# Kernel tuning notes

Hardware: AMD Instinct MI355X
Metric: run time of the kernel (lower is better)

Reference implementation:

```python
import jax, jax.numpy as jnp
import numpy as np

CODEBOOK_SIZE = 1024
CODEWORD_SIZE = 256
BETA = 0.1
N_INIT = 1  # embedding ~ U(-1/n, 1/n)


def setup_inputs() -> dict:
    key = jax.random.key(0)
    kx, ke = jax.random.split(key)
    x = jax.random.normal(kx, (16, 4096, CODEWORD_SIZE), dtype=jnp.float32)
    embedding = jax.random.uniform(
        ke, (CODEBOOK_SIZE, CODEWORD_SIZE), dtype=jnp.float32,
        minval=-1.0 / N_INIT, maxval=1.0 / N_INIT)
    return {"x": x, "embedding": embedding}


def reference(x, embedding):
    dist = (jnp.sum(x * x, axis=2, keepdims=True)
            + jnp.sum(embedding * embedding, axis=1)
            - 2.0 * jnp.einsum('btd,kd->btk', x, embedding))
    indexes = jnp.argmin(dist, axis=2)              # [B,T] int
    values = jnp.take(embedding, indexes, axis=0)   # gather == one_hot @ embedding
    sg = jax.lax.stop_gradient
    loss1 = jnp.mean((sg(x) - values) ** 2)         # codebook loss
    loss2 = jnp.mean((x - sg(values)) ** 2)         # commitment loss
    loss = loss1 + BETA * loss2
    values_st = x + sg(values - x)                  # straight-through
    return values_st, indexes, loss
```

## Files before the change

### kernel.cpp

```cpp
#include <hip/hip_runtime.h>
#include <stdint.h>


#define BT    65536
#define D     256
#define KCB   1024
#define BM    256
#define BN    128
#define BK    32

typedef float    f32x4 __attribute__((ext_vector_type(4)));
typedef _Float16 f16x8 __attribute__((ext_vector_type(8)));

#define GLOAD_LDS16(g, l) \
  __builtin_amdgcn_global_load_lds((const __attribute__((address_space(1))) void*)(g), \
                                   (__attribute__((address_space(3))) void*)(l), 16, 0, 0)

__global__ __launch_bounds__(256) void split_e_kernel(const float* __restrict__ E,
                                                      _Float16* __restrict__ Eh,
                                                      _Float16* __restrict__ El,
                                                      float* __restrict__ enorm,
                                                      float* __restrict__ out_loss) {
    if (blockIdx.x == 0 && threadIdx.x == 0) *out_loss = 0.f;
    const int r = blockIdx.x * 8 + (threadIdx.x >> 5);
    const size_t i0 = (size_t)r * D + (threadIdx.x & 31) * 8;
    float4 v0 = *(const float4*)(E + i0);
    float4 v1 = *(const float4*)(E + i0 + 4);
    float v[8] = {v0.x, v0.y, v0.z, v0.w, v1.x, v1.y, v1.z, v1.w};
    f16x8 h, l;
    float s = 0.f;
    #pragma unroll
    for (int j = 0; j < 8; ++j) {
        _Float16 hh = (_Float16)v[j];
        h[j] = hh;
        l[j] = (_Float16)(v[j] - (float)hh);
        s += v[j] * v[j];
    }
    *(f16x8*)(Eh + i0) = h;
    *(f16x8*)(El + i0) = l;
    #pragma unroll
    for (int off = 1; off < 32; off <<= 1) s += __shfl_xor(s, off, 64);
    if ((threadIdx.x & 31) == 0) enorm[r] = s;
}

__global__ __launch_bounds__(512, 2) void vq_mfma_kernel(
    const float* __restrict__ X,
    const _Float16* __restrict__ Eh, const _Float16* __restrict__ El,
    const float* __restrict__ enorm, const float* __restrict__ E,
    float* __restrict__ out_vals, float* __restrict__ out_idx,
    float* __restrict__ out_loss) {
    __shared__ __align__(16) char Bmem[8 * BN * BK * 2];
    __shared__ float s_en[KCB];
    __shared__ float s_bd[BM];
    __shared__ int   s_bi[BM];
    __shared__ float s_red[8];

    float*    const Xs = (float*)Bmem;
    _Float16* const BB = (_Float16*)Bmem;

    const int tid  = threadIdx.x;
    const int w    = tid >> 6;
    const int lane = tid & 63;
    const int quad = lane >> 4;
    const int l16  = lane & 15;
    const int sxa  = l16 & 7;
    const int row0 = blockIdx.x * BM;

    const int sb_row = lane >> 2;
    const int sb_off = ((((lane & 3) - (lane >> 3)) & 3) << 3);
    const int kob = ((quad + ((l16 >> 1) & 3)) & 3) << 3;

    auto STAGE_PH = [&](int buf, int step) {
        const int col0 = (step >> 2) * BN;
        const int kb0  = (step & 3) * (2 * BK);
        #pragma unroll
        for (int h = 0; h < 2; ++h) {
            const int gr = col0 + w * 16 + sb_row;
            const size_t gb = (size_t)gr * D + kb0 + h * BK + sb_off;
            GLOAD_LDS16(Eh + gb, BB + (buf * 4 + h * 2 + 0) * (BN * BK) + w * 512);
            GLOAD_LDS16(El + gb, BB + (buf * 4 + h * 2 + 1) * (BN * BK) + w * 512);
        }
    };

    s_en[tid]       = enorm[tid];
    s_en[tid + 512] = enorm[tid + 512];

    f16x8 pah[2][8], pal[2][8];
    float xs = 0.f;
    for (int p = 0; p < 4; ++p) {
        #pragma unroll
        for (int rr = 0; rr < 8; ++rr) {
            const int sr = w * 8 + rr;
            const int gr = row0 + p * 64 + sr;
            GLOAD_LDS16(X + (size_t)gr * D + ((lane ^ rr) << 2), &Xs[sr * D]);
        }
        asm volatile("s_waitcnt vmcnt(0) lgkmcnt(0)" ::: "memory");
        __builtin_amdgcn_s_barrier();
        if ((w >> 1) == p) {
            const int srb = (w & 1) * 32;
            #pragma unroll
            for (int i = 0; i < 2; ++i) {
                const float* rp = &Xs[(srb + i * 16 + l16) * D];
                #pragma unroll
                for (int kc = 0; kc < 8; ++kc) {
                    const int c0 = kc * 8 + quad * 2;
                    const f32x4 v0 = *(const f32x4*)(rp + (((c0)     ^ sxa) << 2));
                    const f32x4 v1 = *(const f32x4*)(rp + (((c0 | 1) ^ sxa) << 2));
                    const float f[8] = {v0.x, v0.y, v0.z, v0.w, v1.x, v1.y, v1.z, v1.w};
                    #pragma unroll
                    for (int e = 0; e < 8; ++e) {
                        const _Float16 hh = (_Float16)f[e];
                        pah[i][kc][e] = hh;
                        pal[i][kc][e] = (_Float16)(f[e] - (float)hh);
                        xs += f[e] * f[e];
                    }
                }
            }
        }
        __builtin_amdgcn_s_barrier();
    }

    float rb_d[2][4];
    int   rb_i[2][4];
    #pragma unroll
    for (int i = 0; i < 2; ++i)
        #pragma unroll
        for (int r = 0; r < 4; ++r) { rb_d[i][r] = 3.4e38f; rb_i[i][r] = 0; }
    f32x4 acc[2][8];

    STAGE_PH(0, 0);
    for (int nt = 0; nt < 8; ++nt) {
        const int col0 = nt * BN;
        #pragma unroll
        for (int q = 0; q < 4; ++q) {
            const int cur = q & 1;
            if (nt == 7 && q == 3) {
                asm volatile("s_waitcnt vmcnt(0)" ::: "memory");
            } else {
                STAGE_PH(cur ^ 1, nt * 4 + q + 1);
                asm volatile("s_waitcnt vmcnt(4)" ::: "memory");
            }
            __builtin_amdgcn_s_barrier();

            if (q == 0) {
                #pragma unroll
                for (int i = 0; i < 2; ++i)
                    #pragma unroll
                    for (int j = 0; j < 8; ++j) acc[i][j] = (f32x4)0.0f;
            }

            #pragma unroll
            for (int sub = 0; sub < 2; ++sub) {
                const int kc = q * 2 + sub;
                const _Float16* Bh = BB + (cur * 4 + sub * 2 + 0) * (BN * BK);
                const _Float16* Bl = BB + (cur * 4 + sub * 2 + 1) * (BN * BK);
                __builtin_amdgcn_s_setprio(1);
                #pragma unroll
                for (int j = 0; j < 8; ++j) {
                    const int n = (j * 16 + l16) * BK + kob;
                    const f16x8 bh = *(const f16x8*)&Bh[n];
                    const f16x8 bl = *(const f16x8*)&Bl[n];
                    #pragma unroll
                    for (int i = 0; i < 2; ++i) {
                        acc[i][j] = __builtin_amdgcn_mfma_f32_16x16x32_f16(pah[i][kc], bh, acc[i][j], 0, 0, 0);
                        acc[i][j] = __builtin_amdgcn_mfma_f32_16x16x32_f16(pal[i][kc], bh, acc[i][j], 0, 0, 0);
                        acc[i][j] = __builtin_amdgcn_mfma_f32_16x16x32_f16(pah[i][kc], bl, acc[i][j], 0, 0, 0);
                    }
                }
                __builtin_amdgcn_s_setprio(0);
            }

            if (q == 3) {
                #pragma unroll
                for (int j = 0; j < 8; ++j) {
                    const int c = col0 + j * 16 + l16;
                    const float en = s_en[c];
                    #pragma unroll
                    for (int i = 0; i < 2; ++i)
                        #pragma unroll
                        for (int r = 0; r < 4; ++r) {
                            const float sd = en - 2.0f * acc[i][j][r];
                            if (sd < rb_d[i][r]) { rb_d[i][r] = sd; rb_i[i][r] = c; }
                        }
                }
            }
            __builtin_amdgcn_s_barrier();
        }
    }

    #pragma unroll
    for (int off = 1; off < 16; off <<= 1) {
        #pragma unroll
        for (int i = 0; i < 2; ++i)
            #pragma unroll
            for (int r = 0; r < 4; ++r) {
                const float od = __shfl_xor(rb_d[i][r], off, 64);
                const int   oi = __shfl_xor(rb_i[i][r], off, 64);
                if (od < rb_d[i][r] || (od == rb_d[i][r] && oi < rb_i[i][r])) {
                    rb_d[i][r] = od; rb_i[i][r] = oi;
                }
            }
    }
    if (l16 == 0) {
        #pragma unroll
        for (int i = 0; i < 2; ++i)
            #pragma unroll
            for (int r = 0; r < 4; ++r) {
                const int m = w * 32 + i * 16 + quad * 4 + r;
                s_bd[m] = rb_d[i][r]; s_bi[m] = rb_i[i][r];
            }
    }
    __syncthreads();

    float part = xs;
    if (tid < BM) {
        out_idx[row0 + tid] = (float)s_bi[tid];
        part += s_bd[tid];
    }

    const int col = tid & 255;
    const int sub = tid >> 8;
    #pragma unroll 4
    for (int it = 0; it < BM / 2; ++it) {
        const int r  = it * 2 + sub;
        const int bi = s_bi[r];
        out_vals[(size_t)(row0 + r) * D + col] = E[(size_t)bi * D + col];
    }

    #pragma unroll
    for (int off = 1; off < 64; off <<= 1) part += __shfl_xor(part, off, 64);
    if (lane == 0) s_red[w] = part;
    __syncthreads();
    if (tid == 0) {
        float tot = 0.f;
        #pragma unroll
        for (int i = 0; i < 8; ++i) tot += s_red[i];
        atomicAdd(out_loss, tot * (1.1f / 16777216.f));
    }
}

extern "C" void kernel_launch(void* const* d_in, const int* in_sizes, int n_in,
                              void* d_out, int out_size, void* d_ws, size_t ws_size,
                              hipStream_t stream) {
    const float* X = (const float*)d_in[0];
    const float* E = (const float*)d_in[1];
    float* out      = (float*)d_out;
    float* out_vals = out;
    float* out_idx  = out + (size_t)BT * D;
    float* out_loss = out + (size_t)BT * D + BT;

    char* ws = (char*)d_ws;
    _Float16* Eh    = (_Float16*)ws;
    _Float16* El    = Eh + (size_t)KCB * D;
    float*    enorm = (float*)(El + (size_t)KCB * D);
    (void)ws_size; (void)n_in; (void)in_sizes; (void)out_size;

    split_e_kernel<<<KCB / 8, 256, 0, stream>>>(E, Eh, El, enorm, out_loss);
    vq_mfma_kernel<<<BT / BM, 512, 0, stream>>>(X, Eh, El, enorm, E,
                                                out_vals, out_idx, out_loss);
}
```

Measured before the change: 189.9 us.

## Halve row tile to 128 with 4-wave blocks and double-buffer X staging

Shrinks each block to 128 rows and 256 threads (4 waves), which doubles the grid to 512 blocks. The codebook staging is split so each wave loads two chunks. X prologue loads are now double-buffered across two LDS regions so the next 32-row slab loads while the current one is converted to fp16 hi/lo fragments. The enorm load is moved to the end of the prologue. This should improve load balance over the CUs and overlap the prologue, but each block streams the full codebook for half as many rows, which doubles total codebook traffic per output row.

```diff
diff --git a/kernel.cpp b/kernel.cpp
--- a/kernel.cpp
+++ b/kernel.cpp
@@ -5,7 +5,7 @@
 #define BT    65536
 #define D     256
 #define KCB   1024
-#define BM    256
+#define BM    128
 #define BN    128
 #define BK    32
 
@@ -43,7 +43,7 @@
     if ((threadIdx.x & 31) == 0) enorm[r] = s;
 }
 
-__global__ __launch_bounds__(512, 2) void vq_mfma_kernel(
+__global__ __launch_bounds__(256, 2) void vq_mfma_kernel(
     const float* __restrict__ X,
     const _Float16* __restrict__ Eh, const _Float16* __restrict__ El,
     const float* __restrict__ enorm, const float* __restrict__ E,
@@ -53,10 +53,11 @@
     __shared__ float s_en[KCB];
     __shared__ float s_bd[BM];
     __shared__ int   s_bi[BM];
-    __shared__ float s_red[8];
-
-    float*    const Xs = (float*)Bmem;
-    _Float16* const BB = (_Float16*)Bmem;
+    __shared__ float s_red[4];
+
+    _Float16* const BB  = (_Float16*)Bmem;
+    float*    const Xs0 = (float*)Bmem;
+    float*    const Xs1 = (float*)(Bmem + 32 * 1024);
 
     const int tid  = threadIdx.x;
     const int w    = tid >> 6;
@@ -74,33 +75,47 @@
         const int col0 = (step >> 2) * BN;
         const int kb0  = (step & 3) * (2 * BK);
         #pragma unroll
-        for (int h = 0; h < 2; ++h) {
-            const int gr = col0 + w * 16 + sb_row;
-            const size_t gb = (size_t)gr * D + kb0 + h * BK + sb_off;
-            GLOAD_LDS16(Eh + gb, BB + (buf * 4 + h * 2 + 0) * (BN * BK) + w * 512);
-            GLOAD_LDS16(El + gb, BB + (buf * 4 + h * 2 + 1) * (BN * BK) + w * 512);
-        }
+        for (int h = 0; h < 2; ++h)
+            #pragma unroll
+            for (int t = 0; t < 2; ++t) {
+                const int chunk = w * 2 + t;
+                const int gr = col0 + chunk * 16 + sb_row;
+                const size_t gb = (size_t)gr * D + kb0 + h * BK + sb_off;
+                GLOAD_LDS16(Eh + gb, BB + (buf * 4 + h * 2 + 0) * (BN * BK) + chunk * 512);
+                GLOAD_LDS16(El + gb, BB + (buf * 4 + h * 2 + 1) * (BN * BK) + chunk * 512);
+            }
     };
 
-    s_en[tid]       = enorm[tid];
-    s_en[tid + 512] = enorm[tid + 512];
+    auto STAGE_X = [&](int buf, int p) {
+        float* Xs = buf ? Xs1 : Xs0;
+        #pragma unroll
+        for (int rr = 0; rr < 8; ++rr) {
+            const int sr = w * 8 + rr;
+            const int gr = row0 + p * 32 + sr;
+            GLOAD_LDS16(X + (size_t)gr * D + ((lane ^ rr) << 2), &Xs[sr * D]);
+        }
+    };
 
     f16x8 pah[2][8], pal[2][8];
     float xs = 0.f;
+    STAGE_X(0, 0);
+    #pragma unroll
     for (int p = 0; p < 4; ++p) {
-        #pragma unroll
-        for (int rr = 0; rr < 8; ++rr) {
-            const int sr = w * 8 + rr;
-            const int gr = row0 + p * 64 + sr;
-            GLOAD_LDS16(X + (size_t)gr * D + ((lane ^ rr) << 2), &Xs[sr * D]);
-        }
-        asm volatile("s_waitcnt vmcnt(0) lgkmcnt(0)" ::: "memory");
+        if (p < 3) {
+            STAGE_X((p + 1) & 1, p + 1);
+            asm volatile("s_waitcnt vmcnt(8)" ::: "memory");
+        } else {
+            asm volatile("s_waitcnt vmcnt(0)" ::: "memory");
+            #pragma unroll
+            for (int t = 0; t < 4; ++t) s_en[tid + t * 256] = enorm[tid + t * 256];
+            asm volatile("s_waitcnt vmcnt(0) lgkmcnt(0)" ::: "memory");
+        }
         __builtin_amdgcn_s_barrier();
-        if ((w >> 1) == p) {
-            const int srb = (w & 1) * 32;
+        if (w == p) {
+            const float* Xs = (p & 1) ? Xs1 : Xs0;
             #pragma unroll
             for (int i = 0; i < 2; ++i) {
-                const float* rp = &Xs[(srb + i * 16 + l16) * D];
+                const float* rp = &Xs[(i * 16 + l16) * D];
                 #pragma unroll
                 for (int kc = 0; kc < 8; ++kc) {
                     const int c0 = kc * 8 + quad * 2;
@@ -138,7 +153,7 @@
                 asm volatile("s_waitcnt vmcnt(0)" ::: "memory");
             } else {
                 STAGE_PH(cur ^ 1, nt * 4 + q + 1);
-                asm volatile("s_waitcnt vmcnt(4)" ::: "memory");
+                asm volatile("s_waitcnt vmcnt(8)" ::: "memory");
             }
             __builtin_amdgcn_s_barrier();
 
@@ -218,13 +233,10 @@
         part += s_bd[tid];
     }
 
-    const int col = tid & 255;
-    const int sub = tid >> 8;
     #pragma unroll 4
-    for (int it = 0; it < BM / 2; ++it) {
-        const int r  = it * 2 + sub;
+    for (int r = 0; r < BM; ++r) {
         const int bi = s_bi[r];
-        out_vals[(size_t)(row0 + r) * D + col] = E[(size_t)bi * D + col];
+        out_vals[(size_t)(row0 + r) * D + tid] = E[(size_t)bi * D + tid];
     }
 
     #pragma unroll
@@ -232,9 +244,7 @@
     if (lane == 0) s_red[w] = part;
     __syncthreads();
     if (tid == 0) {
-        float tot = 0.f;
-        #pragma unroll
-        for (int i = 0; i < 8; ++i) tot += s_red[i];
+        const float tot = s_red[0] + s_red[1] + s_red[2] + s_red[3];
         atomicAdd(out_loss, tot * (1.1f / 16777216.f));
     }
 }
@@ -256,6 +266,6 @@
     (void)ws_size; (void)n_in; (void)in_sizes; (void)out_size;
 
     split_e_kernel<<<KCB / 8, 256, 0, stream>>>(E, Eh, El, enorm, out_loss);
-    vq_mfma_kernel<<<BT / BM, 512, 0, stream>>>(X, Eh, El, enorm, E,
+    vq_mfma_kernel<<<BT / BM, 256, 0, stream>>>(X, Eh, El, enorm, E,
                                                 out_vals, out_idx, out_loss);
 }
```

After: 200.0 us. 5.3% more time.
